# Optimization experiments

Measured on AMD Instinct MI355X. Metric: run time of the kernel, lower is better.

## Reference

```python
import jax, jax.numpy as jnp
import numpy as np

N_SRC1, N_DST1, N_DST2 = 500000, 100000, 20000
IN_F, H_F, N_CLS = 128, 128, 16
E1, E2 = 2000000, 1000000


def setup_inputs() -> dict:
    key = jax.random.key(0)
    ks = jax.random.split(key, 12)
    inp = {
        "x": jax.random.normal(ks[0], (N_SRC1, IN_F), dtype=jnp.float32),
        "src1": jax.random.randint(ks[1], (E1,), 0, N_SRC1, dtype=jnp.int64) if False else jax.random.randint(ks[1], (E1,), 0, N_SRC1),
        "dst1": jax.random.randint(ks[2], (E1,), 0, N_DST1),
        "w1": jax.random.uniform(ks[3], (E1,), dtype=jnp.float32),
        "src2": jax.random.randint(ks[4], (E2,), 0, N_DST1),
        "dst2": jax.random.randint(ks[5], (E2,), 0, N_DST2),
        "w2": jax.random.uniform(ks[6], (E2,), dtype=jnp.float32),
        # SAGEConv params: fc_self (no bias), fc_neigh (+ bias), per DGL
        "W_self1": jax.random.normal(ks[7], (IN_F, H_F), dtype=jnp.float32) / np.sqrt(IN_F),
        "W_neigh1": jax.random.normal(ks[8], (IN_F, H_F), dtype=jnp.float32) / np.sqrt(IN_F),
        "b1": jnp.zeros((H_F,), dtype=jnp.float32),
        "W_self2": jax.random.normal(ks[9], (H_F, N_CLS), dtype=jnp.float32) / np.sqrt(H_F),
        "W_neigh2": jax.random.normal(ks[10], (H_F, N_CLS), dtype=jnp.float32) / np.sqrt(H_F),
        "b2": jnp.zeros((N_CLS,), dtype=jnp.float32),
    }
    return inp


def _sage_mean(h_src, h_dst, src, dst, w, W_self, W_neigh, b, n_dst):
    # message: edge_weight * src feature; aggregate: mean over in-edges of dst
    m = h_src[src] * w[:, None]                             # [E, F]
    s = jax.ops.segment_sum(m, dst, num_segments=n_dst)     # [n_dst, F]
    deg = jax.ops.segment_sum(jnp.ones_like(w), dst, num_segments=n_dst)
    neigh = s / jnp.maximum(deg, 1.0)[:, None]
    return h_dst @ W_self + neigh @ W_neigh + b


def reference(x, src1, dst1, w1, src2, dst2, w2,
              W_self1, W_neigh1, b1, W_self2, W_neigh2, b2):
    h_dst = x[:N_DST1]
    h = _sage_mean(x, h_dst, src1, dst1, w1, W_self1, W_neigh1, b1, N_DST1)
    h = jax.nn.relu(h)
    h_dst2 = h[:N_DST2]
    out = _sage_mean(h, h_dst2, src2, dst2, w2, W_self2, W_neigh2, b2, N_DST2)
    return jax.nn.log_softmax(out, axis=1)
```

## Files before the change

kernel.cpp:

```cpp
#include <hip/hip_runtime.h>

#define NSRC1 500000
#define NDST1 100000
#define NDST2 20000
#define NE1   2000000
#define NE2   1000000
#define F     128
#define NCLS  16
#define C1    56
#define C2    128
#define CONV_BLKS 4096

#define TILE_A 4096
#define NT1 ((NE1 + TILE_A - 1) / TILE_A)
#define NT2 ((NE2 + TILE_A - 1) / TILE_A)
#define BINS1 196
#define BINS2 157
#define CAP1 11264
#define CAP2 7168

typedef float vf4 __attribute__((ext_vector_type(4)));
typedef short short8 __attribute__((ext_vector_type(8)));
typedef float f32x4 __attribute__((ext_vector_type(4)));
typedef unsigned short vus8 __attribute__((ext_vector_type(8)));

#define OFF_BINCUR 0
#define OFF_CNT1   4096
#define OFF_CNT2   404096
#define OFF_WSW    484352
#define OFF_W2SW   549888
#define OFF_SLOT1  554240
#define OFF_G      554240
#define OFF_HSM    6954240
#define OFF_SLOT2  22954240
#define OFF_BIN1   33194240
#define OFF_BIN2   50856192
#define OFF_XB     59859200

__device__ __forceinline__ unsigned short f2bf(float f) {
    unsigned u = __float_as_uint(f);
    u = (u + 0x7FFFu + ((u >> 16) & 1u)) >> 16;
    return (unsigned short)u;
}
__device__ __forceinline__ float bfu(unsigned short h) {
    return __uint_as_float(((unsigned)h) << 16);
}

__global__ __launch_bounds__(256) void prep0_kernel(
    const float* __restrict__ Ws1, const float* __restrict__ Wn1,
    const float* __restrict__ Wn2,
    short8* __restrict__ wsw, short8* __restrict__ w2sw,
    int* __restrict__ binCur)
{
    int wb = blockIdx.x, tid = threadIdx.x;
    if (wb < 16) {
        int e = wb * 256 + tid;
        int l = e & 63, st = e >> 6;
        int t = st & 7, s = st >> 3;
        short8 o;
#pragma unroll
        for (int i = 0; i < 8; ++i) {
            int k = s * 32 + (l >> 4) * 8 + i;
            int n = t * 16 + (l & 15);
            float v = (k < F) ? Ws1[k * F + n] : Wn1[(k - F) * F + n];
            o[i] = (short)f2bf(v);
        }
        wsw[e] = o;
    } else if (wb == 16) {
        int l = tid & 63, s2 = tid >> 6;
        short8 o;
#pragma unroll
        for (int i = 0; i < 8; ++i) {
            int k = s2 * 32 + (l >> 4) * 8 + i;
            o[i] = (short)f2bf(Wn2[k * NCLS + (l & 15)]);
        }
        w2sw[s2 * 64 + l] = o;
    } else {
        for (int i = tid; i < 1024; i += 256) binCur[i] = 0;
    }
}

__global__ __launch_bounds__(256) void prepA_kernel(
    const int* __restrict__ dst1, const int* __restrict__ src1,
    const float* __restrict__ w1,
    const int* __restrict__ dst2, const int* __restrict__ src2,
    const float* __restrict__ w2,
    int* __restrict__ binCur, int2* __restrict__ bin1, int2* __restrict__ bin2,
    const vf4* __restrict__ x4, ushort4* __restrict__ xb)
{
    int tid = threadIdx.x;
    if (blockIdx.x < NT1 + NT2) {
        __shared__ int hist[BINS1];
        __shared__ int basearr[BINS1];
        bool isL2 = blockIdx.x >= NT1;
        int tile = isL2 ? blockIdx.x - NT1 : blockIdx.x;
        const int nb    = isL2 ? BINS2 : BINS1;
        const int shift = isL2 ? 7 : 9;
        const int sb    = isL2 ? 17 : 19;
        const int nE    = isL2 ? NE2 : NE1;
        const int cap   = isL2 ? CAP2 : CAP1;
        const int* dst   = isL2 ? dst2 : dst1;
        const int* src   = isL2 ? src2 : src1;
        const float* w   = isL2 ? w2 : w1;
        int2* bout       = isL2 ? bin2 : bin1;
        int* cur         = binCur + (isL2 ? BINS1 : 0);

        for (int i = tid; i < nb; i += 256) hist[i] = 0;
        __syncthreads();

        int base = tile * TILE_A;
        int key[16]; float wv[16]; int bn[16];
#pragma unroll
        for (int k = 0; k < 16; ++k) {
            int t = base + k * 256 + tid;
            if (t < nE) {
                int d = dst[t];
                int b = d >> shift;
                bn[k] = b;
                key[k] = src[t] | ((d & ((1 << shift) - 1)) << sb);
                wv[k] = w[t];
                atomicAdd(&hist[b], 1);
            } else bn[k] = -1;
        }
        __syncthreads();
        for (int i = tid; i < nb; i += 256) {
            int c = hist[i];
            basearr[i] = c ? atomicAdd(&cur[i], c) : 0;
            hist[i] = 0;
        }
        __syncthreads();
#pragma unroll
        for (int k = 0; k < 16; ++k) {
            if (bn[k] >= 0) {
                int r = atomicAdd(&hist[bn[k]], 1);
                int p = basearr[bn[k]] + r;
                if (p < cap)
                    bout[(size_t)bn[k] * cap + p] = make_int2(key[k], __float_as_int(wv[k]));
            }
        }
    } else {
        const long n = (long)NSRC1 * F / 4;
        const long stride = (long)CONV_BLKS * 256;
        long i = (long)(blockIdx.x - NT1 - NT2) * 256 + tid;
        while (i + 3 * stride < n) {
            vf4 v0 = __builtin_nontemporal_load(&x4[i]);
            vf4 v1 = __builtin_nontemporal_load(&x4[i + stride]);
            vf4 v2 = __builtin_nontemporal_load(&x4[i + 2 * stride]);
            vf4 v3 = __builtin_nontemporal_load(&x4[i + 3 * stride]);
            ushort4 o0, o1, o2, o3;
            o0.x = f2bf(v0.x); o0.y = f2bf(v0.y); o0.z = f2bf(v0.z); o0.w = f2bf(v0.w);
            o1.x = f2bf(v1.x); o1.y = f2bf(v1.y); o1.z = f2bf(v1.z); o1.w = f2bf(v1.w);
            o2.x = f2bf(v2.x); o2.y = f2bf(v2.y); o2.z = f2bf(v2.z); o2.w = f2bf(v2.w);
            o3.x = f2bf(v3.x); o3.y = f2bf(v3.y); o3.z = f2bf(v3.z); o3.w = f2bf(v3.w);
            xb[i] = o0;
            xb[i + stride] = o1;
            xb[i + 2 * stride] = o2;
            xb[i + 3 * stride] = o3;
            i += 4 * stride;
        }
        for (; i < n; i += stride) {
            vf4 v = __builtin_nontemporal_load(&x4[i]);
            ushort4 o;
            o.x = f2bf(v.x); o.y = f2bf(v.y); o.z = f2bf(v.z); o.w = f2bf(v.w);
            xb[i] = o;
        }
    }
}

__global__ __launch_bounds__(256) void binB_kernel(
    const int* __restrict__ binCur,
    const int2* __restrict__ bin1, const int2* __restrict__ bin2,
    unsigned* __restrict__ slot1, unsigned* __restrict__ slot2,
    int* __restrict__ cnt1, int* __restrict__ cnt2)
{
    __shared__ int pos[512];
    int tid = threadIdx.x;
    if (blockIdx.x < BINS1) {
        int b = blockIdx.x;
        for (int i = tid; i < 512; i += 256) pos[i] = 0;
        __syncthreads();
        int n = min(binCur[b], CAP1);
        const int2* ptr = bin1 + (size_t)b * CAP1;
        for (int i = tid; i < n; i += 256) {
            int2 rec = ptr[i];
            int dlow = ((unsigned)rec.x) >> 19;
            int s = rec.x & 0x7FFFF;
            float wf = __int_as_float(rec.y);
            int p = atomicAdd(&pos[dlow], 1);
            if (p < C1) {
                unsigned wq = min((unsigned)(wf * 8192.0f), 8191u);
                slot1[(size_t)((b << 9) | dlow) * C1 + p] = ((unsigned)s << 13) | wq;
            }
        }
        __syncthreads();
        for (int i = tid; i < 512; i += 256) {
            int d = (b << 9) + i;
            if (d < NDST1) cnt1[d] = pos[i];
        }
    } else {
        int b = blockIdx.x - BINS1;
        if (tid < 128) pos[tid] = 0;
        __syncthreads();
        int n = min(binCur[BINS1 + b], CAP2);
        const int2* ptr = bin2 + (size_t)b * CAP2;
        for (int i = tid; i < n; i += 256) {
            int2 rec = ptr[i];
            int dlow = ((unsigned)rec.x) >> 17;
            int s = rec.x & 0x1FFFF;
            float wf = __int_as_float(rec.y);
            int p = atomicAdd(&pos[dlow], 1);
            if (p < C2) {
                unsigned wq = min((unsigned)(wf * 32768.0f), 32767u);
                slot2[(((size_t)((b << 7) | dlow)) << 7) + p] = ((unsigned)s << 15) | wq;
            }
        }
        __syncthreads();
        if (tid < 128) {
            int d = (b << 7) + tid;
            if (d < NDST2) cnt2[d] = pos[tid];
        }
    }
}

__global__ __launch_bounds__(256) void dense1f_kernel(
    const short8* __restrict__ xb8, const vus8* __restrict__ xbv,
    const unsigned* __restrict__ slot1, const int* __restrict__ cnt1,
    const short8* __restrict__ wsw, const short8* __restrict__ w2sw,
    const float* __restrict__ b1, float* __restrict__ hsmall,
    float* __restrict__ g)
{
    __shared__ short lds_a[64 * 256];
    short8* la8 = (short8*)lds_a;

    int tid = threadIdx.x;
    int wv = tid >> 6, l = tid & 63;
    int r0 = blockIdx.x * 64;

    for (int it = tid; it < 1024; it += 256) {
        int r = it >> 4, c = it & 15;
        int grow = min(r0 + r, NDST1 - 1);
        la8[r * 32 + (c ^ (r & 7))] = xb8[(size_t)grow * 16 + c];
    }

    {
        int grp = tid >> 4, j = tid & 15;
        for (int rr = 0; rr < 4; ++rr) {
            int rloc = rr * 16 + grp;
            int row = min(r0 + rloc, NDST1 - 1);
            int deg = cnt1[row];
            int n = min(deg, C1);
            const unsigned* bucket = slot1 + (size_t)row * C1;
            float a[8] = {0.f, 0.f, 0.f, 0.f, 0.f, 0.f, 0.f, 0.f};
            int nb = (n + 7) >> 3;
            unsigned e[8];
            if (nb > 0) {
#pragma unroll
                for (int q = 0; q < 8; ++q) e[q] = bucket[min(q, n - 1)];
            }
            for (int bi = 0; bi < nb; ++bi) {
                int base = bi * 8;
                float wq[8];
                vus8 v[8];
#pragma unroll
                for (int q = 0; q < 8; ++q) {
                    wq[q] = (base + q < n) ? ((float)(e[q] & 8191u) + 0.5f) * (1.0f / 8192.0f) : 0.f;
                    v[q] = xbv[(size_t)(e[q] >> 13) * 16 + j];
                }
                if (bi + 1 < nb) {
                    int nbase = base + 8;
#pragma unroll
                    for (int q = 0; q < 8; ++q) e[q] = bucket[min(nbase + q, n - 1)];
                }
#pragma unroll
                for (int q = 0; q < 8; ++q) {
#pragma unroll
                    for (int k = 0; k < 8; ++k)
                        a[k] += bfu(v[q][k]) * wq[q];
                }
            }
            float invd = 1.0f / fmaxf((float)deg, 1.0f);
            short8 o;
#pragma unroll
            for (int k = 0; k < 8; ++k) o[k] = (short)f2bf(a[k] * invd);
            la8[rloc * 32 + ((16 + j) ^ (rloc & 7))] = o;
        }
    }
    __syncthreads();

    int lq = l >> 4;
    int lrow = wv * 16 + (l & 15);
    int lbase = lrow * 32;
    int lkey = lrow & 7;

    f32x4 acc[8];
#pragma unroll
    for (int t = 0; t < 8; ++t) acc[t] = (f32x4){0.f, 0.f, 0.f, 0.f};

#pragma unroll
    for (int s = 0; s < 8; ++s) {
        short8 af = la8[lbase + ((s * 4 + lq) ^ lkey)];
#pragma unroll
        for (int t = 0; t < 8; ++t) {
            short8 bf_ = wsw[(s * 8 + t) * 64 + l];
            acc[t] = __builtin_amdgcn_mfma_f32_16x16x32_bf16(af, bf_, acc[t], 0, 0, 0);
        }
    }
    __syncthreads();

    int orow_base = r0 + wv * 16 + lq * 4;
#pragma unroll
    for (int t = 0; t < 8; ++t) {
        float bv = b1[t * 16 + (l & 15)];
        int col = t * 16 + (l & 15);
        int chunk = col >> 3;
#pragma unroll
        for (int r = 0; r < 4; ++r) {
            float hv = fmaxf(acc[t][r] + bv, 0.f);
            int lr = wv * 16 + lq * 4 + r;
            lds_a[lr * 256 + ((chunk ^ (lr & 7)) << 3) + (col & 7)] = (short)f2bf(hv);
            int orow = orow_base + r;
            if (orow < NDST2) hsmall[(size_t)orow * F + col] = hv;
        }
    }
    __syncthreads();

    f32x4 acc2 = (f32x4){0.f, 0.f, 0.f, 0.f};
#pragma unroll
    for (int s2 = 0; s2 < 4; ++s2) {
        short8 af = la8[lbase + ((s2 * 4 + lq) ^ lkey)];
        short8 bf_ = w2sw[s2 * 64 + l];
        acc2 = __builtin_amdgcn_mfma_f32_16x16x32_bf16(af, bf_, acc2, 0, 0, 0);
    }
#pragma unroll
    for (int r = 0; r < 4; ++r) {
        int orow = orow_base + r;
        if (orow < NDST1) g[(size_t)orow * NCLS + (l & 15)] = acc2[r];
    }
}

__global__ __launch_bounds__(256) void dense2_kernel(
    const float* __restrict__ hsmall, const float* __restrict__ g,
    const unsigned* __restrict__ slot2, const int* __restrict__ cnt2,
    const float* __restrict__ Ws2, const float* __restrict__ b2,
    float* __restrict__ out)
{
    __shared__ float ws[F * NCLS];
    __shared__ float hsh[16][F + 1];
    int tid = threadIdx.x;
    for (int i = tid; i < F * NCLS / 4; i += 256)
        ((float4*)ws)[i] = ((const float4*)Ws2)[i];
    int r0 = blockIdx.x * 16;
    for (int it = tid; it < 16 * 32; it += 256) {
        int r = it >> 5, c = it & 31;
        *(float4*)&hsh[r][c * 4] = ((const float4*)hsmall)[(size_t)(r0 + r) * 32 + c];
    }
    __syncthreads();

    int grp = tid >> 4, j = tid & 15;
    int row = r0 + grp;
    int deg = cnt2[row];
    int n = min(deg, C2);
    const unsigned* bucket = slot2 + ((size_t)row << 7);
    float acc = 0.f;
    int nb = (n + 7) >> 3;
    unsigned e[8];
    if (nb > 0) {
#pragma unroll
        for (int q = 0; q < 8; ++q) e[q] = bucket[min(q, n - 1)];
    }
    for (int bi = 0; bi < nb; ++bi) {
        int base = bi * 8;
        float wq[8], gv[8];
#pragma unroll
        for (int q = 0; q < 8; ++q) {
            wq[q] = (base + q < n) ? ((float)(e[q] & 32767u) + 0.5f) * (1.0f / 32768.0f) : 0.f;
            gv[q] = g[(size_t)(e[q] >> 15) * NCLS + j];
        }
        if (bi + 1 < nb) {
            int nbase = base + 8;
#pragma unroll
            for (int q = 0; q < 8; ++q) e[q] = bucket[min(nbase + q, n - 1)];
        }
#pragma unroll
        for (int q = 0; q < 8; ++q) acc += gv[q] * wq[q];
    }
    float invd = 1.0f / fmaxf((float)deg, 1.0f);
    float v = b2[j] + acc * invd;
#pragma unroll 8
    for (int k = 0; k < F; ++k)
        v += hsh[grp][k] * ws[k * NCLS + j];

    float m = v;
    for (int o = 8; o >= 1; o >>= 1) m = fmaxf(m, __shfl_xor(m, o, 16));
    float s = expf(v - m);
    for (int o = 8; o >= 1; o >>= 1) s += __shfl_xor(s, o, 16);
    out[(size_t)row * NCLS + j] = v - m - logf(s);
}

extern "C" void kernel_launch(void* const* d_in, const int* in_sizes, int n_in,
                              void* d_out, int out_size, void* d_ws, size_t ws_size,
                              hipStream_t stream)
{
    const float* x    = (const float*)d_in[0];
    const int*   src1 = (const int*)d_in[1];
    const int*   dst1 = (const int*)d_in[2];
    const float* w1   = (const float*)d_in[3];
    const int*   src2 = (const int*)d_in[4];
    const int*   dst2 = (const int*)d_in[5];
    const float* w2   = (const float*)d_in[6];
    const float* Ws1  = (const float*)d_in[7];
    const float* Wn1  = (const float*)d_in[8];
    const float* b1   = (const float*)d_in[9];
    const float* Ws2  = (const float*)d_in[10];
    const float* Wn2  = (const float*)d_in[11];
    const float* b2   = (const float*)d_in[12];
    float* out = (float*)d_out;

    char* wsb = (char*)d_ws;
    int*      binCur = (int*)(wsb + OFF_BINCUR);
    int*      cnt1   = (int*)(wsb + OFF_CNT1);
    int*      cnt2   = (int*)(wsb + OFF_CNT2);
    short8*   wsw    = (short8*)(wsb + OFF_WSW);
    short8*   w2sw   = (short8*)(wsb + OFF_W2SW);
    unsigned* slot1  = (unsigned*)(wsb + OFF_SLOT1);
    unsigned* slot2  = (unsigned*)(wsb + OFF_SLOT2);
    int2*     bin1   = (int2*)(wsb + OFF_BIN1);
    int2*     bin2   = (int2*)(wsb + OFF_BIN2);
    float*    g      = (float*)(wsb + OFF_G);
    float*    hsmall = (float*)(wsb + OFF_HSM);
    ushort4*  xb     = (ushort4*)(wsb + OFF_XB);

    prep0_kernel<<<18, 256, 0, stream>>>(Ws1, Wn1, Wn2, wsw, w2sw, binCur);

    prepA_kernel<<<NT1 + NT2 + CONV_BLKS, 256, 0, stream>>>(
        dst1, src1, w1, dst2, src2, w2, binCur, bin1, bin2, (const vf4*)x, xb);

    binB_kernel<<<BINS1 + BINS2, 256, 0, stream>>>(
        binCur, bin1, bin2, slot1, slot2, cnt1, cnt2);

    dense1f_kernel<<<(NDST1 + 63) / 64, 256, 0, stream>>>(
        (const short8*)xb, (const vus8*)xb, slot1, cnt1, wsw, w2sw, b1, hsmall, g);

    dense2_kernel<<<NDST2 / 16, 256, 0, stream>>>(
        hsmall, g, slot2, cnt2, Ws2, b2, out);
}
```

Measured before the change: 249.4 us.

## Stage binned edges in LDS for coalesced writes; move x conversion into second pass

The first binning pass now sorts each tile's edges by bin in shared memory, using a prefix scan and per-bin cursors, and then writes them out contiguously. This replaces scattered per-edge global stores with mostly coalesced runs. The fp32-to-bf16 conversion of x moves from the first pass into the second binning kernel, so it runs alongside the slot-building blocks. dense1f also gains a min-occupancy launch bound of 4, which may cap its register use. Costs are extra LDS (about 45KB per block), lower occupancy in binA, and additional barriers for the scan.

```diff
diff --git a/kernel.cpp b/kernel.cpp
--- a/kernel.cpp
+++ b/kernel.cpp
@@ -80,98 +80,97 @@
     }
 }
 
-__global__ __launch_bounds__(256) void prepA_kernel(
+__global__ __launch_bounds__(256) void binA_kernel(
     const int* __restrict__ dst1, const int* __restrict__ src1,
     const float* __restrict__ w1,
     const int* __restrict__ dst2, const int* __restrict__ src2,
     const float* __restrict__ w2,
-    int* __restrict__ binCur, int2* __restrict__ bin1, int2* __restrict__ bin2,
-    const vf4* __restrict__ x4, ushort4* __restrict__ xb)
-{
+    int* __restrict__ binCur, int2* __restrict__ bin1, int2* __restrict__ bin2)
+{
+    __shared__ int2 staged[TILE_A];
+    __shared__ unsigned short sbin[TILE_A];
+    __shared__ int offA[BINS1];
+    __shared__ int cursor[BINS1];
+    __shared__ int basearr[BINS1];
+    __shared__ int scanbuf[2][256];
+
     int tid = threadIdx.x;
-    if (blockIdx.x < NT1 + NT2) {
-        __shared__ int hist[BINS1];
-        __shared__ int basearr[BINS1];
-        bool isL2 = blockIdx.x >= NT1;
-        int tile = isL2 ? blockIdx.x - NT1 : blockIdx.x;
-        const int nb    = isL2 ? BINS2 : BINS1;
-        const int shift = isL2 ? 7 : 9;
-        const int sb    = isL2 ? 17 : 19;
-        const int nE    = isL2 ? NE2 : NE1;
-        const int cap   = isL2 ? CAP2 : CAP1;
-        const int* dst   = isL2 ? dst2 : dst1;
-        const int* src   = isL2 ? src2 : src1;
-        const float* w   = isL2 ? w2 : w1;
-        int2* bout       = isL2 ? bin2 : bin1;
-        int* cur         = binCur + (isL2 ? BINS1 : 0);
-
-        for (int i = tid; i < nb; i += 256) hist[i] = 0;
+    bool isL2 = blockIdx.x >= NT1;
+    int tile = isL2 ? blockIdx.x - NT1 : blockIdx.x;
+    const int nb    = isL2 ? BINS2 : BINS1;
+    const int shift = isL2 ? 7 : 9;
+    const int sb    = isL2 ? 17 : 19;
+    const int nE    = isL2 ? NE2 : NE1;
+    const int cap   = isL2 ? CAP2 : CAP1;
+    const int* dst   = isL2 ? dst2 : dst1;
+    const int* src   = isL2 ? src2 : src1;
+    const float* w   = isL2 ? w2 : w1;
+    int2* bout       = isL2 ? bin2 : bin1;
+    int* cur         = binCur + (isL2 ? BINS1 : 0);
+
+    for (int i = tid; i < nb; i += 256) cursor[i] = 0;
+    __syncthreads();
+
+    int base = tile * TILE_A;
+    int tileCnt = min(TILE_A, nE - base);
+    int key[16]; float wv[16]; int bn[16];
+#pragma unroll
+    for (int k = 0; k < 16; ++k) {
+        int t = base + k * 256 + tid;
+        if (t < nE) {
+            int d = dst[t];
+            int b = d >> shift;
+            bn[k] = b;
+            key[k] = src[t] | ((d & ((1 << shift) - 1)) << sb);
+            wv[k] = w[t];
+            atomicAdd(&cursor[b], 1);
+        } else bn[k] = -1;
+    }
+    __syncthreads();
+
+    int hv = (tid < nb) ? cursor[tid] : 0;
+    scanbuf[0][tid] = hv;
+    __syncthreads();
+    int curb = 0;
+    for (int off = 1; off < 256; off <<= 1) {
+        int t = scanbuf[curb][tid];
+        if (tid >= off) t += scanbuf[curb][tid - off];
+        scanbuf[curb ^ 1][tid] = t;
+        curb ^= 1;
         __syncthreads();
-
-        int base = tile * TILE_A;
-        int key[16]; float wv[16]; int bn[16];
-#pragma unroll
-        for (int k = 0; k < 16; ++k) {
-            int t = base + k * 256 + tid;
-            if (t < nE) {
-                int d = dst[t];
-                int b = d >> shift;
-                bn[k] = b;
-                key[k] = src[t] | ((d & ((1 << shift) - 1)) << sb);
-                wv[k] = w[t];
-                atomicAdd(&hist[b], 1);
-            } else bn[k] = -1;
-        }
-        __syncthreads();
-        for (int i = tid; i < nb; i += 256) {
-            int c = hist[i];
-            basearr[i] = c ? atomicAdd(&cur[i], c) : 0;
-            hist[i] = 0;
-        }
-        __syncthreads();
-#pragma unroll
-        for (int k = 0; k < 16; ++k) {
-            if (bn[k] >= 0) {
-                int r = atomicAdd(&hist[bn[k]], 1);
-                int p = basearr[bn[k]] + r;
-                if (p < cap)
-                    bout[(size_t)bn[k] * cap + p] = make_int2(key[k], __float_as_int(wv[k]));
-            }
-        }
-    } else {
-        const long n = (long)NSRC1 * F / 4;
-        const long stride = (long)CONV_BLKS * 256;
-        long i = (long)(blockIdx.x - NT1 - NT2) * 256 + tid;
-        while (i + 3 * stride < n) {
-            vf4 v0 = __builtin_nontemporal_load(&x4[i]);
-            vf4 v1 = __builtin_nontemporal_load(&x4[i + stride]);
-            vf4 v2 = __builtin_nontemporal_load(&x4[i + 2 * stride]);
-            vf4 v3 = __builtin_nontemporal_load(&x4[i + 3 * stride]);
-            ushort4 o0, o1, o2, o3;
-            o0.x = f2bf(v0.x); o0.y = f2bf(v0.y); o0.z = f2bf(v0.z); o0.w = f2bf(v0.w);
-            o1.x = f2bf(v1.x); o1.y = f2bf(v1.y); o1.z = f2bf(v1.z); o1.w = f2bf(v1.w);
-            o2.x = f2bf(v2.x); o2.y = f2bf(v2.y); o2.z = f2bf(v2.z); o2.w = f2bf(v2.w);
-            o3.x = f2bf(v3.x); o3.y = f2bf(v3.y); o3.z = f2bf(v3.z); o3.w = f2bf(v3.w);
-            xb[i] = o0;
-            xb[i + stride] = o1;
-            xb[i + 2 * stride] = o2;
-            xb[i + 3 * stride] = o3;
-            i += 4 * stride;
-        }
-        for (; i < n; i += stride) {
-            vf4 v = __builtin_nontemporal_load(&x4[i]);
-            ushort4 o;
-            o.x = f2bf(v.x); o.y = f2bf(v.y); o.z = f2bf(v.z); o.w = f2bf(v.w);
-            xb[i] = o;
-        }
-    }
-}
-
-__global__ __launch_bounds__(256) void binB_kernel(
+    }
+    int exc = scanbuf[curb][tid] - hv;
+    if (tid < nb) {
+        offA[tid] = exc;
+        basearr[tid] = hv ? atomicAdd(&cur[tid], hv) : 0;
+    }
+    __syncthreads();
+    if (tid < nb) cursor[tid] = exc;
+    __syncthreads();
+
+#pragma unroll
+    for (int k = 0; k < 16; ++k) {
+        if (bn[k] >= 0) {
+            int p = atomicAdd(&cursor[bn[k]], 1);
+            staged[p] = make_int2(key[k], __float_as_int(wv[k]));
+            sbin[p] = (unsigned short)bn[k];
+        }
+    }
+    __syncthreads();
+
+    for (int i = tid; i < tileCnt; i += 256) {
+        int b = sbin[i];
+        int pos = basearr[b] + (i - offA[b]);
+        if (pos < cap) bout[(size_t)b * cap + pos] = staged[i];
+    }
+}
+
+__global__ __launch_bounds__(256) void convB_kernel(
     const int* __restrict__ binCur,
     const int2* __restrict__ bin1, const int2* __restrict__ bin2,
     unsigned* __restrict__ slot1, unsigned* __restrict__ slot2,
-    int* __restrict__ cnt1, int* __restrict__ cnt2)
+    int* __restrict__ cnt1, int* __restrict__ cnt2,
+    const vf4* __restrict__ x4, ushort4* __restrict__ xb)
 {
     __shared__ int pos[512];
     int tid = threadIdx.x;
@@ -197,7 +196,7 @@
             int d = (b << 9) + i;
             if (d < NDST1) cnt1[d] = pos[i];
         }
-    } else {
+    } else if (blockIdx.x < BINS1 + BINS2) {
         int b = blockIdx.x - BINS1;
         if (tid < 128) pos[tid] = 0;
         __syncthreads();
@@ -219,10 +218,36 @@
             int d = (b << 7) + tid;
             if (d < NDST2) cnt2[d] = pos[tid];
         }
-    }
-}
-
-__global__ __launch_bounds__(256) void dense1f_kernel(
+    } else {
+        const long n = (long)NSRC1 * F / 4;
+        const long stride = (long)CONV_BLKS * 256;
+        long i = (long)(blockIdx.x - BINS1 - BINS2) * 256 + tid;
+        while (i + 3 * stride < n) {
+            vf4 v0 = __builtin_nontemporal_load(&x4[i]);
+            vf4 v1 = __builtin_nontemporal_load(&x4[i + stride]);
+            vf4 v2 = __builtin_nontemporal_load(&x4[i + 2 * stride]);
+            vf4 v3 = __builtin_nontemporal_load(&x4[i + 3 * stride]);
+            ushort4 o0, o1, o2, o3;
+            o0.x = f2bf(v0.x); o0.y = f2bf(v0.y); o0.z = f2bf(v0.z); o0.w = f2bf(v0.w);
+            o1.x = f2bf(v1.x); o1.y = f2bf(v1.y); o1.z = f2bf(v1.z); o1.w = f2bf(v1.w);
+            o2.x = f2bf(v2.x); o2.y = f2bf(v2.y); o2.z = f2bf(v2.z); o2.w = f2bf(v2.w);
+            o3.x = f2bf(v3.x); o3.y = f2bf(v3.y); o3.z = f2bf(v3.z); o3.w = f2bf(v3.w);
+            xb[i] = o0;
+            xb[i + stride] = o1;
+            xb[i + 2 * stride] = o2;
+            xb[i + 3 * stride] = o3;
+            i += 4 * stride;
+        }
+        for (; i < n; i += stride) {
+            vf4 v = __builtin_nontemporal_load(&x4[i]);
+            ushort4 o;
+            o.x = f2bf(v.x); o.y = f2bf(v.y); o.z = f2bf(v.z); o.w = f2bf(v.w);
+            xb[i] = o;
+        }
+    }
+}
+
+__global__ __launch_bounds__(256, 4) void dense1f_kernel(
     const short8* __restrict__ xb8, const vus8* __restrict__ xbv,
     const unsigned* __restrict__ slot1, const int* __restrict__ cnt1,
     const short8* __restrict__ wsw, const short8* __restrict__ w2sw,
@@ -432,11 +457,11 @@
 
     prep0_kernel<<<18, 256, 0, stream>>>(Ws1, Wn1, Wn2, wsw, w2sw, binCur);
 
-    prepA_kernel<<<NT1 + NT2 + CONV_BLKS, 256, 0, stream>>>(
-        dst1, src1, w1, dst2, src2, w2, binCur, bin1, bin2, (const vf4*)x, xb);
-
-    binB_kernel<<<BINS1 + BINS2, 256, 0, stream>>>(
-        binCur, bin1, bin2, slot1, slot2, cnt1, cnt2);
+    binA_kernel<<<NT1 + NT2, 256, 0, stream>>>(
+        dst1, src1, w1, dst2, src2, w2, binCur, bin1, bin2);
+
+    convB_kernel<<<BINS1 + BINS2 + CONV_BLKS, 256, 0, stream>>>(
+        binCur, bin1, bin2, slot1, slot2, cnt1, cnt2, (const vf4*)x, xb);
 
     dense1f_kernel<<<(NDST1 + 63) / 64, 256, 0, stream>>>(
         (const short8*)xb, (const vus8*)xb, slot1, cnt1, wsw, w2sw, b1, hsmall, g);
```

Result: faster. 230.3 us (-7.6%).

## Split x bf16 conversion across binning kernels and move weight prep

Applied to the files above, without the earlier changes.

Splits the fp32-to-bf16 conversion of x into two halves. The first half runs alongside the edge-tile binning in the first pass, and the second half runs alongside the per-bin slot packing in the second pass. The point is to overlap the bandwidth-bound conversion with the atomic-heavy binning in both kernels rather than only one. Weight swizzling moves into the second kernel, leaving a single-block zeroing kernel. Adds launch_bounds occupancy hint 4 to dense1f, which may cap registers and cause spills.

```diff
diff --git a/kernel.cpp b/kernel.cpp
--- a/kernel.cpp
+++ b/kernel.cpp
@@ -9,7 +9,6 @@
 #define NCLS  16
 #define C1    56
 #define C2    128
-#define CONV_BLKS 4096
 
 #define TILE_A 4096
 #define NT1 ((NE1 + TILE_A - 1) / TILE_A)
@@ -18,6 +17,9 @@
 #define BINS2 157
 #define CAP1 11264
 #define CAP2 7168
+#define CONV_BLKS 2048
+#define NV4 16000000L
+#define NV4_HALF 8000000L
 
 typedef float vf4 __attribute__((ext_vector_type(4)));
 typedef short short8 __attribute__((ext_vector_type(8)));
@@ -46,41 +48,41 @@
     return __uint_as_float(((unsigned)h) << 16);
 }
 
-__global__ __launch_bounds__(256) void prep0_kernel(
-    const float* __restrict__ Ws1, const float* __restrict__ Wn1,
-    const float* __restrict__ Wn2,
-    short8* __restrict__ wsw, short8* __restrict__ w2sw,
-    int* __restrict__ binCur)
-{
-    int wb = blockIdx.x, tid = threadIdx.x;
-    if (wb < 16) {
-        int e = wb * 256 + tid;
-        int l = e & 63, st = e >> 6;
-        int t = st & 7, s = st >> 3;
-        short8 o;
-#pragma unroll
-        for (int i = 0; i < 8; ++i) {
-            int k = s * 32 + (l >> 4) * 8 + i;
-            int n = t * 16 + (l & 15);
-            float v = (k < F) ? Ws1[k * F + n] : Wn1[(k - F) * F + n];
-            o[i] = (short)f2bf(v);
-        }
-        wsw[e] = o;
-    } else if (wb == 16) {
-        int l = tid & 63, s2 = tid >> 6;
-        short8 o;
-#pragma unroll
-        for (int i = 0; i < 8; ++i) {
-            int k = s2 * 32 + (l >> 4) * 8 + i;
-            o[i] = (short)f2bf(Wn2[k * NCLS + (l & 15)]);
-        }
-        w2sw[s2 * 64 + l] = o;
-    } else {
-        for (int i = tid; i < 1024; i += 256) binCur[i] = 0;
-    }
-}
-
-__global__ __launch_bounds__(256) void prepA_kernel(
+__device__ __forceinline__ void conv_range(
+    const vf4* __restrict__ x4, ushort4* __restrict__ xb,
+    long i, long lim)
+{
+    const long stride = (long)CONV_BLKS * 256;
+    while (i + 3 * stride < lim) {
+        vf4 v0 = __builtin_nontemporal_load(&x4[i]);
+        vf4 v1 = __builtin_nontemporal_load(&x4[i + stride]);
+        vf4 v2 = __builtin_nontemporal_load(&x4[i + 2 * stride]);
+        vf4 v3 = __builtin_nontemporal_load(&x4[i + 3 * stride]);
+        ushort4 o0, o1, o2, o3;
+        o0.x = f2bf(v0.x); o0.y = f2bf(v0.y); o0.z = f2bf(v0.z); o0.w = f2bf(v0.w);
+        o1.x = f2bf(v1.x); o1.y = f2bf(v1.y); o1.z = f2bf(v1.z); o1.w = f2bf(v1.w);
+        o2.x = f2bf(v2.x); o2.y = f2bf(v2.y); o2.z = f2bf(v2.z); o2.w = f2bf(v2.w);
+        o3.x = f2bf(v3.x); o3.y = f2bf(v3.y); o3.z = f2bf(v3.z); o3.w = f2bf(v3.w);
+        xb[i] = o0;
+        xb[i + stride] = o1;
+        xb[i + 2 * stride] = o2;
+        xb[i + 3 * stride] = o3;
+        i += 4 * stride;
+    }
+    for (; i < lim; i += stride) {
+        vf4 v = __builtin_nontemporal_load(&x4[i]);
+        ushort4 o;
+        o.x = f2bf(v.x); o.y = f2bf(v.y); o.z = f2bf(v.z); o.w = f2bf(v.w);
+        xb[i] = o;
+    }
+}
+
+__global__ __launch_bounds__(256) void prep0_kernel(int* __restrict__ binCur)
+{
+    for (int i = threadIdx.x; i < 1024; i += 256) binCur[i] = 0;
+}
+
+__global__ __launch_bounds__(256) void prepAC_kernel(
     const int* __restrict__ dst1, const int* __restrict__ src1,
     const float* __restrict__ w1,
     const int* __restrict__ dst2, const int* __restrict__ src2,
@@ -88,10 +90,10 @@
     int* __restrict__ binCur, int2* __restrict__ bin1, int2* __restrict__ bin2,
     const vf4* __restrict__ x4, ushort4* __restrict__ xb)
 {
+    __shared__ int hist[BINS1];
+    __shared__ int basearr[BINS1];
     int tid = threadIdx.x;
     if (blockIdx.x < NT1 + NT2) {
-        __shared__ int hist[BINS1];
-        __shared__ int basearr[BINS1];
         bool isL2 = blockIdx.x >= NT1;
         int tile = isL2 ? blockIdx.x - NT1 : blockIdx.x;
         const int nb    = isL2 ? BINS2 : BINS1;
@@ -139,39 +141,20 @@
             }
         }
     } else {
-        const long n = (long)NSRC1 * F / 4;
-        const long stride = (long)CONV_BLKS * 256;
         long i = (long)(blockIdx.x - NT1 - NT2) * 256 + tid;
-        while (i + 3 * stride < n) {
-            vf4 v0 = __builtin_nontemporal_load(&x4[i]);
-            vf4 v1 = __builtin_nontemporal_load(&x4[i + stride]);
-            vf4 v2 = __builtin_nontemporal_load(&x4[i + 2 * stride]);
-            vf4 v3 = __builtin_nontemporal_load(&x4[i + 3 * stride]);
-            ushort4 o0, o1, o2, o3;
-            o0.x = f2bf(v0.x); o0.y = f2bf(v0.y); o0.z = f2bf(v0.z); o0.w = f2bf(v0.w);
-            o1.x = f2bf(v1.x); o1.y = f2bf(v1.y); o1.z = f2bf(v1.z); o1.w = f2bf(v1.w);
-            o2.x = f2bf(v2.x); o2.y = f2bf(v2.y); o2.z = f2bf(v2.z); o2.w = f2bf(v2.w);
-            o3.x = f2bf(v3.x); o3.y = f2bf(v3.y); o3.z = f2bf(v3.z); o3.w = f2bf(v3.w);
-            xb[i] = o0;
-            xb[i + stride] = o1;
-            xb[i + 2 * stride] = o2;
-            xb[i + 3 * stride] = o3;
-            i += 4 * stride;
-        }
-        for (; i < n; i += stride) {
-            vf4 v = __builtin_nontemporal_load(&x4[i]);
-            ushort4 o;
-            o.x = f2bf(v.x); o.y = f2bf(v.y); o.z = f2bf(v.z); o.w = f2bf(v.w);
-            xb[i] = o;
-        }
-    }
-}
-
-__global__ __launch_bounds__(256) void binB_kernel(
+        conv_range(x4, xb, i, NV4_HALF);
+    }
+}
+
+__global__ __launch_bounds__(256) void binBC_kernel(
     const int* __restrict__ binCur,
     const int2* __restrict__ bin1, const int2* __restrict__ bin2,
     unsigned* __restrict__ slot1, unsigned* __restrict__ slot2,
-    int* __restrict__ cnt1, int* __restrict__ cnt2)
+    int* __restrict__ cnt1, int* __restrict__ cnt2,
+    const float* __restrict__ Ws1, const float* __restrict__ Wn1,
+    const float* __restrict__ Wn2,
+    short8* __restrict__ wsw, short8* __restrict__ w2sw,
+    const vf4* __restrict__ x4, ushort4* __restrict__ xb)
 {
     __shared__ int pos[512];
     int tid = threadIdx.x;
@@ -197,7 +180,7 @@
             int d = (b << 9) + i;
             if (d < NDST1) cnt1[d] = pos[i];
         }
-    } else {
+    } else if (blockIdx.x < BINS1 + BINS2) {
         int b = blockIdx.x - BINS1;
         if (tid < 128) pos[tid] = 0;
         __syncthreads();
@@ -219,10 +202,38 @@
             int d = (b << 7) + tid;
             if (d < NDST2) cnt2[d] = pos[tid];
         }
-    }
-}
-
-__global__ __launch_bounds__(256) void dense1f_kernel(
+    } else if (blockIdx.x < BINS1 + BINS2 + 17) {
+        int wb = blockIdx.x - BINS1 - BINS2;
+        if (wb < 16) {
+            int e = wb * 256 + tid;
+            int l = e & 63, st = e >> 6;
+            int t = st & 7, s = st >> 3;
+            short8 o;
+#pragma unroll
+            for (int i = 0; i < 8; ++i) {
+                int k = s * 32 + (l >> 4) * 8 + i;
+                int n = t * 16 + (l & 15);
+                float v = (k < F) ? Ws1[k * F + n] : Wn1[(k - F) * F + n];
+                o[i] = (short)f2bf(v);
+            }
+            wsw[e] = o;
+        } else {
+            int l = tid & 63, s2 = tid >> 6;
+            short8 o;
+#pragma unroll
+            for (int i = 0; i < 8; ++i) {
+                int k = s2 * 32 + (l >> 4) * 8 + i;
+                o[i] = (short)f2bf(Wn2[k * NCLS + (l & 15)]);
+            }
+            w2sw[s2 * 64 + l] = o;
+        }
+    } else {
+        long i = NV4_HALF + (long)(blockIdx.x - BINS1 - BINS2 - 17) * 256 + tid;
+        conv_range(x4, xb, i, NV4);
+    }
+}
+
+__global__ __launch_bounds__(256, 4) void dense1f_kernel(
     const short8* __restrict__ xb8, const vus8* __restrict__ xbv,
     const unsigned* __restrict__ slot1, const int* __restrict__ cnt1,
     const short8* __restrict__ wsw, const short8* __restrict__ w2sw,
@@ -430,13 +441,15 @@
     float*    hsmall = (float*)(wsb + OFF_HSM);
     ushort4*  xb     = (ushort4*)(wsb + OFF_XB);
 
-    prep0_kernel<<<18, 256, 0, stream>>>(Ws1, Wn1, Wn2, wsw, w2sw, binCur);
-
-    prepA_kernel<<<NT1 + NT2 + CONV_BLKS, 256, 0, stream>>>(
-        dst1, src1, w1, dst2, src2, w2, binCur, bin1, bin2, (const vf4*)x, xb);
-
-    binB_kernel<<<BINS1 + BINS2, 256, 0, stream>>>(
-        binCur, bin1, bin2, slot1, slot2, cnt1, cnt2);
+    prep0_kernel<<<1, 256, 0, stream>>>(binCur);
+
+    prepAC_kernel<<<NT1 + NT2 + CONV_BLKS, 256, 0, stream>>>(
+        dst1, src1, w1, dst2, src2, w2, binCur, bin1, bin2,
+        (const vf4*)x, xb);
+
+    binBC_kernel<<<BINS1 + BINS2 + 17 + CONV_BLKS, 256, 0, stream>>>(
+        binCur, bin1, bin2, slot1, slot2, cnt1, cnt2,
+        Ws1, Wn1, Wn2, wsw, w2sw, (const vf4*)x, xb);
 
     dense1f_kernel<<<(NDST1 + 63) / 64, 256, 0, stream>>>(
         (const short8*)xb, (const vus8*)xb, slot1, cnt1, wsw, w2sw, b1, hsmall, g);
```

After: 255.0 us. 2.2% more time.
